# Kernel tuning notes

Hardware: AMD Instinct MI355X
Metric: run time of the kernel (lower is better)

## Reference

```python
import jax, jax.numpy as jnp
import numpy as np

B, D, R = 16, 1024, 100  # batch, input_dim==output_dim, measurement rounds


def setup_inputs() -> dict:
    key = jax.random.key(0)
    k = jax.random.split(key, 6)
    x = jax.random.normal(k[0], (B, 1, D), dtype=jnp.float32)
    quantum_weights = jax.random.normal(k[1], (D, D), dtype=jnp.float32) * 0.1
    quantum_phase = jax.random.normal(k[2], (D, D), dtype=jnp.float32) * np.float32(np.pi)
    entanglement_matrix = jax.random.normal(k[3], (D, D), dtype=jnp.float32) * 0.1
    bound = np.float32(1.0 / np.sqrt(D))  # torch nn.Linear default init range
    gate_W = jax.random.uniform(k[4], (R, D, D), minval=-bound, maxval=bound, dtype=jnp.float32)
    gate_b = jax.random.uniform(k[5], (R, D), minval=-bound, maxval=bound, dtype=jnp.float32)
    return {"x": x, "quantum_weights": quantum_weights, "quantum_phase": quantum_phase,
            "entanglement_matrix": entanglement_matrix, "gate_W": gate_W, "gate_b": gate_b}


def reference(x, quantum_weights, quantum_phase, entanglement_matrix, gate_W, gate_b):
    # quantum_x = complex(x*cos(phase), x*sin(phase)); since quantum_weights and
    # entanglement_matrix are real, .real of (quantum_x @ W @ E) equals the real
    # branch only -> the sin branch never reaches the output (identical math).
    real = (x * jnp.cos(quantum_phase))            # (B, D, D) via broadcast
    entangled_real = real @ quantum_weights @ entanglement_matrix  # (B, D, D)
    # mean over R measurement gates: gate_r(y) = y @ W_r^T + b_r (torch Linear)
    out = jnp.einsum('bij,rkj->bik', entangled_real, gate_W) / R + jnp.mean(gate_b, axis=0)
    return out
```

## Files before the change

### kernel.cpp

```cpp
#include <hip/hip_runtime.h>
#include <hip/hip_fp16.h>
#include <math.h>

#define B_SZ 16
#define D 1024
#define R_SZ 100
#define DD (D * D)

typedef _Float16 half8 __attribute__((ext_vector_type(8)));
typedef _Float16 half4v __attribute__((ext_vector_type(4)));
typedef float float4v __attribute__((ext_vector_type(4)));

__global__ __launch_bounds__(256) void reduce_w_kernel(
    const float* __restrict__ gW, _Float16* __restrict__ Wsumh) {
    const int idx = blockIdx.x * blockDim.x + threadIdx.x;
    const float4* p = (const float4*)gW;
    float4 s = make_float4(0.f, 0.f, 0.f, 0.f);
#pragma unroll 4
    for (int r = 0; r < R_SZ; ++r) {
        float4 v = p[idx + r * (DD / 4)];
        s.x += v.x; s.y += v.y; s.z += v.z; s.w += v.w;
    }
    const float inv = 1.0f / (float)R_SZ;
    half4v h;
    h[0] = (_Float16)(s.x * inv); h[1] = (_Float16)(s.y * inv);
    h[2] = (_Float16)(s.z * inv); h[3] = (_Float16)(s.w * inv);
    *(half4v*)&Wsumh[idx * 4] = h;
}

__global__ __launch_bounds__(256) void reduce_b_kernel(
    const float* __restrict__ gb, float* __restrict__ bmean) {
    const int k = blockIdx.x * blockDim.x + threadIdx.x;
    float s = 0.f;
#pragma unroll 4
    for (int r = 0; r < R_SZ; ++r) s += gb[r * D + k];
    bmean[k] = s * (1.0f / (float)R_SZ);
}

__global__ __launch_bounds__(256) void cvt_f2h_kernel(
    const float* __restrict__ in, _Float16* __restrict__ out) {
    const int i = blockIdx.x * blockDim.x + threadIdx.x;
    float4 v = ((const float4*)in)[i];
    half4v h;
    h[0] = (_Float16)v.x; h[1] = (_Float16)v.y;
    h[2] = (_Float16)v.z; h[3] = (_Float16)v.w;
    *(half4v*)&out[i * 4] = h;
}

__global__ __launch_bounds__(256) void cos_h_kernel(
    const float* __restrict__ ph, _Float16* __restrict__ out) {
    const int i = blockIdx.x * blockDim.x + threadIdx.x;
    float4 v = ((const float4*)ph)[i];
    half4v h;
    h[0] = (_Float16)cosf(v.x); h[1] = (_Float16)cosf(v.y);
    h[2] = (_Float16)cosf(v.z); h[3] = (_Float16)cosf(v.w);
    *(half4v*)&out[i * 4] = h;
}

__global__ __launch_bounds__(256) void cvt_x_kernel(
    const float* __restrict__ x, _Float16* __restrict__ xh) {
    const int i = blockIdx.x * blockDim.x + threadIdx.x;
    xh[i] = (_Float16)x[i];
}

__global__ __launch_bounds__(256) void tcvt_kernel(
    const float* __restrict__ in, _Float16* __restrict__ out) {
    __shared__ float t[32][33];
    const int tx = threadIdx.x, ty = threadIdx.y;
    int x = blockIdx.x * 32 + tx;
    int y0 = blockIdx.y * 32;
#pragma unroll
    for (int j = 0; j < 32; j += 8) t[ty + j][tx] = in[(y0 + ty + j) * D + x];
    __syncthreads();
    int xo = blockIdx.y * 32 + tx;
    int yo = blockIdx.x * 32;
#pragma unroll
    for (int j = 0; j < 32; j += 8)
        out[(yo + ty + j) * D + xo] = (_Float16)t[tx][ty + j];
}

template <bool SCALE_BIAS>
__global__ __launch_bounds__(256) void mfma_gemm_bt(
    const _Float16* __restrict__ A, const _Float16* __restrict__ BT,
    const _Float16* __restrict__ xh, const float* __restrict__ bias,
    void* __restrict__ Cout) {
    __shared__ __align__(16) _Float16 As[128 * 32];
    __shared__ __align__(16) _Float16 Bs[128 * 32];
    const int tid = threadIdx.x;
    const int wid = tid >> 6;
    const int lane = tid & 63;
    const int brow = blockIdx.y * 128;
    const int bcol = blockIdx.x * 128;
    const int batch = SCALE_BIAS ? blockIdx.z : 0;
    const _Float16* xb = SCALE_BIAS ? (xh + batch * D) : (const _Float16*)nullptr;

    const int s_r = tid >> 2;
    const int s_k = (tid & 3) * 8;
    const int wr = wid >> 1, wc = wid & 1;
    const int fr = lane & 15;
    const int fk = (lane >> 4) * 8;

    float4v acc[4][4] = {};

    for (int k0 = 0; k0 < D; k0 += 32) {
        __syncthreads();
        const _Float16* ga0 = A + (size_t)(brow + s_r) * D + k0 + s_k;
        const _Float16* ga1 = A + (size_t)(brow + 64 + s_r) * D + k0 + s_k;
        const _Float16* gb0 = BT + (size_t)(bcol + s_r) * D + k0 + s_k;
        const _Float16* gb1 = BT + (size_t)(bcol + 64 + s_r) * D + k0 + s_k;
        __builtin_amdgcn_global_load_lds(
            (const __attribute__((address_space(1))) void*)ga0,
            (__attribute__((address_space(3))) void*)(As + wid * 512), 16, 0, 0);
        __builtin_amdgcn_global_load_lds(
            (const __attribute__((address_space(1))) void*)ga1,
            (__attribute__((address_space(3))) void*)(As + 2048 + wid * 512), 16, 0, 0);
        __builtin_amdgcn_global_load_lds(
            (const __attribute__((address_space(1))) void*)gb0,
            (__attribute__((address_space(3))) void*)(Bs + wid * 512), 16, 0, 0);
        __builtin_amdgcn_global_load_lds(
            (const __attribute__((address_space(1))) void*)gb1,
            (__attribute__((address_space(3))) void*)(Bs + 2048 + wid * 512), 16, 0, 0);
        __syncthreads();

        half8 xf;
        if constexpr (SCALE_BIAS) xf = *(const half8*)&xb[k0 + fk];
        half8 a[4], b[4];
#pragma unroll
        for (int m = 0; m < 4; ++m)
            a[m] = *(const half8*)&As[(wr * 64 + m * 16 + fr) * 32 + fk];
#pragma unroll
        for (int n = 0; n < 4; ++n) {
            b[n] = *(const half8*)&Bs[(wc * 64 + n * 16 + fr) * 32 + fk];
            if constexpr (SCALE_BIAS) b[n] = b[n] * xf;
        }
#pragma unroll
        for (int m = 0; m < 4; ++m)
#pragma unroll
            for (int n = 0; n < 4; ++n)
                acc[m][n] = __builtin_amdgcn_mfma_f32_16x16x32_f16(
                    a[m], b[n], acc[m][n], 0, 0, 0);
    }

    const int crow = (lane >> 4) * 4;
    const int ccol = lane & 15;
    if constexpr (SCALE_BIAS) {
        float* outb = (float*)Cout + (size_t)batch * DD;
#pragma unroll
        for (int n = 0; n < 4; ++n) {
            const int gn = bcol + wc * 64 + n * 16 + ccol;
            const float bm = bias[gn];
#pragma unroll
            for (int m = 0; m < 4; ++m) {
                const int gm0 = brow + wr * 64 + m * 16 + crow;
#pragma unroll
                for (int r = 0; r < 4; ++r)
                    outb[(size_t)(gm0 + r) * D + gn] = acc[m][n][r] + bm;
            }
        }
    } else {
        _Float16* outh = (_Float16*)Cout;
#pragma unroll
        for (int n = 0; n < 4; ++n) {
            const int gn = bcol + wc * 64 + n * 16 + ccol;
#pragma unroll
            for (int m = 0; m < 4; ++m) {
                const int gm0 = brow + wr * 64 + m * 16 + crow;
#pragma unroll
                for (int r = 0; r < 4; ++r)
                    outh[(size_t)(gm0 + r) * D + gn] = (_Float16)acc[m][n][r];
            }
        }
    }
}

extern "C" void kernel_launch(void* const* d_in, const int* in_sizes, int n_in,
                              void* d_out, int out_size, void* d_ws, size_t ws_size,
                              hipStream_t stream) {
    const float* x  = (const float*)d_in[0];
    const float* qw = (const float*)d_in[1];
    const float* qp = (const float*)d_in[2];
    const float* em = (const float*)d_in[3];
    const float* gW = (const float*)d_in[4];
    const float* gb = (const float*)d_in[5];
    float* out = (float*)d_out;

    _Float16* h = (_Float16*)d_ws;
    _Float16* QWh   = h;
    _Float16* ETh   = h + (1 << 20);
    _Float16* cosCh = h + 2 * (1 << 20);
    _Float16* Wsumh = h + 3 * (1 << 20);
    _Float16* Ph    = h + 4 * (1 << 20);
    _Float16* MTh   = h + 5 * (1 << 20);
    _Float16* xh    = h + 6 * (1 << 20);
    float* bmean    = (float*)(h + 6 * (1 << 20) + 32768);

    reduce_w_kernel<<<DD / 4 / 256, 256, 0, stream>>>(gW, Wsumh);
    reduce_b_kernel<<<D / 256, 256, 0, stream>>>(gb, bmean);
    cvt_f2h_kernel<<<DD / 4 / 256, 256, 0, stream>>>(qw, QWh);
    cos_h_kernel<<<DD / 4 / 256, 256, 0, stream>>>(qp, cosCh);
    tcvt_kernel<<<dim3(32, 32), dim3(32, 8), 0, stream>>>(em, ETh);
    cvt_x_kernel<<<B_SZ * D / 256, 256, 0, stream>>>(x, xh);
    mfma_gemm_bt<false><<<dim3(8, 8), 256, 0, stream>>>(QWh, ETh, nullptr, nullptr, Ph);
    mfma_gemm_bt<false><<<dim3(8, 8), 256, 0, stream>>>(Wsumh, Ph, nullptr, nullptr, MTh);
    mfma_gemm_bt<true><<<dim3(8, 8, B_SZ), 256, 0, stream>>>(cosCh, MTh, xh, bmean, out);
}
```

Before: 685.0 us.

## Fuse preprocessing kernels and overlap gate weight reduction with first GEMM

Merges the six small conversion and reduction kernels into one launch that dispatches by block index. The 100-round gate weight reduction now runs in the same launch as the first D×D GEMM, so the memory-bound reduction can overlap with MFMA work. The two square GEMMs move from 128×128 tiles to 64×64 tiles, giving 256 blocks instead of 64 to fill more CUs. The trade-off is more launch-branch divergence and lower per-block data reuse.

```diff
diff --git a/kernel.cpp b/kernel.cpp
--- a/kernel.cpp
+++ b/kernel.cpp
@@ -11,79 +11,142 @@
 typedef _Float16 half4v __attribute__((ext_vector_type(4)));
 typedef float float4v __attribute__((ext_vector_type(4)));
 
-__global__ __launch_bounds__(256) void reduce_w_kernel(
+__global__ __launch_bounds__(256) void fused_cvt_kernel(
+    const float* __restrict__ qw, const float* __restrict__ qp,
+    const float* __restrict__ em, const float* __restrict__ x,
+    const float* __restrict__ gb,
+    _Float16* __restrict__ QWh, _Float16* __restrict__ cosCh,
+    _Float16* __restrict__ ETh, _Float16* __restrict__ xh,
+    float* __restrict__ bmean) {
+    __shared__ float t[32][33];
+    const int blk = blockIdx.x, tid = threadIdx.x;
+    if (blk < 1024) {
+        const int i = blk * 256 + tid;
+        float4 v = ((const float4*)qw)[i];
+        half4v h;
+        h[0] = (_Float16)v.x; h[1] = (_Float16)v.y;
+        h[2] = (_Float16)v.z; h[3] = (_Float16)v.w;
+        *(half4v*)&QWh[i * 4] = h;
+    } else if (blk < 2048) {
+        const int i = (blk - 1024) * 256 + tid;
+        float4 v = ((const float4*)qp)[i];
+        half4v h;
+        h[0] = (_Float16)cosf(v.x); h[1] = (_Float16)cosf(v.y);
+        h[2] = (_Float16)cosf(v.z); h[3] = (_Float16)cosf(v.w);
+        *(half4v*)&cosCh[i * 4] = h;
+    } else if (blk < 3072) {
+        const int local = blk - 2048;
+        const int bx = local & 31, by = local >> 5;
+        const int tx = tid & 31, ty = tid >> 5;
+#pragma unroll
+        for (int j = 0; j < 32; j += 8)
+            t[ty + j][tx] = em[(by * 32 + ty + j) * D + bx * 32 + tx];
+        __syncthreads();
+#pragma unroll
+        for (int j = 0; j < 32; j += 8)
+            ETh[(size_t)(bx * 32 + ty + j) * D + by * 32 + tx] =
+                (_Float16)t[tx][ty + j];
+    } else if (blk < 3088) {
+        const int i = (blk - 3072) * 256 + tid;
+        float4 v = ((const float4*)x)[i];
+        half4v h;
+        h[0] = (_Float16)v.x; h[1] = (_Float16)v.y;
+        h[2] = (_Float16)v.z; h[3] = (_Float16)v.w;
+        *(half4v*)&xh[i * 4] = h;
+    } else {
+        const int k = (blk - 3088) * 256 + tid;
+        float s = 0.f;
+#pragma unroll 4
+        for (int r = 0; r < R_SZ; ++r) s += gb[r * D + k];
+        bmean[k] = s * (1.0f / (float)R_SZ);
+    }
+}
+
+__device__ __forceinline__ void gemm64_body(
+    const _Float16* __restrict__ A, const _Float16* __restrict__ BT,
+    _Float16* __restrict__ C, int bid, int tid,
+    _Float16* As, _Float16* Bs) {
+    const int wid = tid >> 6, lane = tid & 63;
+    const int brow = (bid >> 4) * 64, bcol = (bid & 15) * 64;
+    const int s_r = tid >> 2, s_k = (tid & 3) * 8;
+    const int wr = wid >> 1, wc = wid & 1;
+    const int fr = lane & 15, fk = (lane >> 4) * 8;
+    float4v acc[2][2] = {};
+    for (int k0 = 0; k0 < D; k0 += 32) {
+        __syncthreads();
+        const _Float16* ga = A + (size_t)(brow + s_r) * D + k0 + s_k;
+        const _Float16* gbp = BT + (size_t)(bcol + s_r) * D + k0 + s_k;
+        __builtin_amdgcn_global_load_lds(
+            (const __attribute__((address_space(1))) void*)ga,
+            (__attribute__((address_space(3))) void*)(As + wid * 512), 16, 0, 0);
+        __builtin_amdgcn_global_load_lds(
+            (const __attribute__((address_space(1))) void*)gbp,
+            (__attribute__((address_space(3))) void*)(Bs + wid * 512), 16, 0, 0);
+        __syncthreads();
+        half8 a[2], b[2];
+        a[0] = *(const half8*)&As[(wr * 32 + fr) * 32 + fk];
+        a[1] = *(const half8*)&As[(wr * 32 + 16 + fr) * 32 + fk];
+        b[0] = *(const half8*)&Bs[(wc * 32 + fr) * 32 + fk];
+        b[1] = *(const half8*)&Bs[(wc * 32 + 16 + fr) * 32 + fk];
+#pragma unroll
+        for (int m = 0; m < 2; ++m)
+#pragma unroll
+            for (int n = 0; n < 2; ++n)
+                acc[m][n] = __builtin_amdgcn_mfma_f32_16x16x32_f16(
+                    a[m], b[n], acc[m][n], 0, 0, 0);
+    }
+    const int crow = (lane >> 4) * 4, ccol = lane & 15;
+#pragma unroll
+    for (int n = 0; n < 2; ++n) {
+        const int gn = bcol + wc * 32 + n * 16 + ccol;
+#pragma unroll
+        for (int m = 0; m < 2; ++m) {
+            const int gm0 = brow + wr * 32 + m * 16 + crow;
+#pragma unroll
+            for (int r = 0; r < 4; ++r)
+                C[(size_t)(gm0 + r) * D + gn] = (_Float16)acc[m][n][r];
+        }
+    }
+}
+
+__global__ __launch_bounds__(256) void mega_pw_kernel(
+    const _Float16* __restrict__ QWh, const _Float16* __restrict__ ETh,
+    _Float16* __restrict__ Ph,
     const float* __restrict__ gW, _Float16* __restrict__ Wsumh) {
-    const int idx = blockIdx.x * blockDim.x + threadIdx.x;
-    const float4* p = (const float4*)gW;
-    float4 s = make_float4(0.f, 0.f, 0.f, 0.f);
+    __shared__ __align__(16) _Float16 As[64 * 32];
+    __shared__ __align__(16) _Float16 Bs[64 * 32];
+    const int tid = threadIdx.x;
+    if (blockIdx.x < 256) {
+        gemm64_body(QWh, ETh, Ph, blockIdx.x, tid, As, Bs);
+    } else {
+        const int idx = (blockIdx.x - 256) * 256 + tid;
+        const float4* p = (const float4*)gW;
+        float4 s = make_float4(0.f, 0.f, 0.f, 0.f);
 #pragma unroll 4
-    for (int r = 0; r < R_SZ; ++r) {
-        float4 v = p[idx + r * (DD / 4)];
-        s.x += v.x; s.y += v.y; s.z += v.z; s.w += v.w;
-    }
-    const float inv = 1.0f / (float)R_SZ;
-    half4v h;
-    h[0] = (_Float16)(s.x * inv); h[1] = (_Float16)(s.y * inv);
-    h[2] = (_Float16)(s.z * inv); h[3] = (_Float16)(s.w * inv);
-    *(half4v*)&Wsumh[idx * 4] = h;
-}
-
-__global__ __launch_bounds__(256) void reduce_b_kernel(
-    const float* __restrict__ gb, float* __restrict__ bmean) {
-    const int k = blockIdx.x * blockDim.x + threadIdx.x;
-    float s = 0.f;
-#pragma unroll 4
-    for (int r = 0; r < R_SZ; ++r) s += gb[r * D + k];
-    bmean[k] = s * (1.0f / (float)R_SZ);
-}
-
-__global__ __launch_bounds__(256) void cvt_f2h_kernel(
-    const float* __restrict__ in, _Float16* __restrict__ out) {
-    const int i = blockIdx.x * blockDim.x + threadIdx.x;
-    float4 v = ((const float4*)in)[i];
-    half4v h;
-    h[0] = (_Float16)v.x; h[1] = (_Float16)v.y;
-    h[2] = (_Float16)v.z; h[3] = (_Float16)v.w;
-    *(half4v*)&out[i * 4] = h;
-}
-
-__global__ __launch_bounds__(256) void cos_h_kernel(
-    const float* __restrict__ ph, _Float16* __restrict__ out) {
-    const int i = blockIdx.x * blockDim.x + threadIdx.x;
-    float4 v = ((const float4*)ph)[i];
-    half4v h;
-    h[0] = (_Float16)cosf(v.x); h[1] = (_Float16)cosf(v.y);
-    h[2] = (_Float16)cosf(v.z); h[3] = (_Float16)cosf(v.w);
-    *(half4v*)&out[i * 4] = h;
-}
-
-__global__ __launch_bounds__(256) void cvt_x_kernel(
-    const float* __restrict__ x, _Float16* __restrict__ xh) {
-    const int i = blockIdx.x * blockDim.x + threadIdx.x;
-    xh[i] = (_Float16)x[i];
-}
-
-__global__ __launch_bounds__(256) void tcvt_kernel(
-    const float* __restrict__ in, _Float16* __restrict__ out) {
-    __shared__ float t[32][33];
-    const int tx = threadIdx.x, ty = threadIdx.y;
-    int x = blockIdx.x * 32 + tx;
-    int y0 = blockIdx.y * 32;
-#pragma unroll
-    for (int j = 0; j < 32; j += 8) t[ty + j][tx] = in[(y0 + ty + j) * D + x];
-    __syncthreads();
-    int xo = blockIdx.y * 32 + tx;
-    int yo = blockIdx.x * 32;
-#pragma unroll
-    for (int j = 0; j < 32; j += 8)
-        out[(yo + ty + j) * D + xo] = (_Float16)t[tx][ty + j];
-}
-
-template <bool SCALE_BIAS>
-__global__ __launch_bounds__(256) void mfma_gemm_bt(
+        for (int r = 0; r < R_SZ; ++r) {
+            float4 v = p[idx + r * (DD / 4)];
+            s.x += v.x; s.y += v.y; s.z += v.z; s.w += v.w;
+        }
+        const float inv = 1.0f / (float)R_SZ;
+        half4v h;
+        h[0] = (_Float16)(s.x * inv); h[1] = (_Float16)(s.y * inv);
+        h[2] = (_Float16)(s.z * inv); h[3] = (_Float16)(s.w * inv);
+        *(half4v*)&Wsumh[idx * 4] = h;
+    }
+}
+
+__global__ __launch_bounds__(256) void gemm64_kernel(
+    const _Float16* __restrict__ A, const _Float16* __restrict__ BT,
+    _Float16* __restrict__ C) {
+    __shared__ __align__(16) _Float16 As[64 * 32];
+    __shared__ __align__(16) _Float16 Bs[64 * 32];
+    gemm64_body(A, BT, C, blockIdx.x, threadIdx.x, As, Bs);
+}
+
+__global__ __launch_bounds__(256) void batched_out_kernel(
     const _Float16* __restrict__ A, const _Float16* __restrict__ BT,
     const _Float16* __restrict__ xh, const float* __restrict__ bias,
-    void* __restrict__ Cout) {
+    float* __restrict__ Cout) {
     __shared__ __align__(16) _Float16 As[128 * 32];
     __shared__ __align__(16) _Float16 Bs[128 * 32];
     const int tid = threadIdx.x;
@@ -91,8 +154,8 @@
     const int lane = tid & 63;
     const int brow = blockIdx.y * 128;
     const int bcol = blockIdx.x * 128;
-    const int batch = SCALE_BIAS ? blockIdx.z : 0;
-    const _Float16* xb = SCALE_BIAS ? (xh + batch * D) : (const _Float16*)nullptr;
+    const int batch = blockIdx.z;
+    const _Float16* xb = xh + batch * D;
 
     const int s_r = tid >> 2;
     const int s_k = (tid & 3) * 8;
@@ -122,8 +185,7 @@
             (__attribute__((address_space(3))) void*)(Bs + 2048 + wid * 512), 16, 0, 0);
         __syncthreads();
 
-        half8 xf;
-        if constexpr (SCALE_BIAS) xf = *(const half8*)&xb[k0 + fk];
+        half8 xf = *(const half8*)&xb[k0 + fk];
         half8 a[4], b[4];
 #pragma unroll
         for (int m = 0; m < 4; ++m)
@@ -131,7 +193,7 @@
 #pragma unroll
         for (int n = 0; n < 4; ++n) {
             b[n] = *(const half8*)&Bs[(wc * 64 + n * 16 + fr) * 32 + fk];
-            if constexpr (SCALE_BIAS) b[n] = b[n] * xf;
+            b[n] = b[n] * xf;
         }
 #pragma unroll
         for (int m = 0; m < 4; ++m)
@@ -143,32 +205,17 @@
 
     const int crow = (lane >> 4) * 4;
     const int ccol = lane & 15;
-    if constexpr (SCALE_BIAS) {
-        float* outb = (float*)Cout + (size_t)batch * DD;
-#pragma unroll
-        for (int n = 0; n < 4; ++n) {
-            const int gn = bcol + wc * 64 + n * 16 + ccol;
-            const float bm = bias[gn];
-#pragma unroll
-            for (int m = 0; m < 4; ++m) {
-                const int gm0 = brow + wr * 64 + m * 16 + crow;
-#pragma unroll
-                for (int r = 0; r < 4; ++r)
-                    outb[(size_t)(gm0 + r) * D + gn] = acc[m][n][r] + bm;
-            }
-        }
-    } else {
-        _Float16* outh = (_Float16*)Cout;
-#pragma unroll
-        for (int n = 0; n < 4; ++n) {
-            const int gn = bcol + wc * 64 + n * 16 + ccol;
-#pragma unroll
-            for (int m = 0; m < 4; ++m) {
-                const int gm0 = brow + wr * 64 + m * 16 + crow;
-#pragma unroll
-                for (int r = 0; r < 4; ++r)
-                    outh[(size_t)(gm0 + r) * D + gn] = (_Float16)acc[m][n][r];
-            }
+    float* outb = Cout + (size_t)batch * DD;
+#pragma unroll
+    for (int n = 0; n < 4; ++n) {
+        const int gn = bcol + wc * 64 + n * 16 + ccol;
+        const float bm = bias[gn];
+#pragma unroll
+        for (int m = 0; m < 4; ++m) {
+            const int gm0 = brow + wr * 64 + m * 16 + crow;
+#pragma unroll
+            for (int r = 0; r < 4; ++r)
+                outb[(size_t)(gm0 + r) * D + gn] = acc[m][n][r] + bm;
         }
     }
 }
@@ -194,13 +241,9 @@
     _Float16* xh    = h + 6 * (1 << 20);
     float* bmean    = (float*)(h + 6 * (1 << 20) + 32768);
 
-    reduce_w_kernel<<<DD / 4 / 256, 256, 0, stream>>>(gW, Wsumh);
-    reduce_b_kernel<<<D / 256, 256, 0, stream>>>(gb, bmean);
-    cvt_f2h_kernel<<<DD / 4 / 256, 256, 0, stream>>>(qw, QWh);
-    cos_h_kernel<<<DD / 4 / 256, 256, 0, stream>>>(qp, cosCh);
-    tcvt_kernel<<<dim3(32, 32), dim3(32, 8), 0, stream>>>(em, ETh);
-    cvt_x_kernel<<<B_SZ * D / 256, 256, 0, stream>>>(x, xh);
-    mfma_gemm_bt<false><<<dim3(8, 8), 256, 0, stream>>>(QWh, ETh, nullptr, nullptr, Ph);
-    mfma_gemm_bt<false><<<dim3(8, 8), 256, 0, stream>>>(Wsumh, Ph, nullptr, nullptr, MTh);
-    mfma_gemm_bt<true><<<dim3(8, 8, B_SZ), 256, 0, stream>>>(cosCh, MTh, xh, bmean, out);
-}
+    fused_cvt_kernel<<<3092, 256, 0, stream>>>(qw, qp, em, x, gb,
+                                               QWh, cosCh, ETh, xh, bmean);
+    mega_pw_kernel<<<1280, 256, 0, stream>>>(QWh, ETh, Ph, gW, Wsumh);
+    gemm64_kernel<<<256, 256, 0, stream>>>(Wsumh, Ph, MTh);
+    batched_out_kernel<<<dim3(8, 8, B_SZ), 256, 0, stream>>>(cosCh, MTh, xh, bmean, out);
+}
```

After: 664.5 us. -3.0%, faster.
